# Optimization experiments

Measured on AMD Instinct MI355X. Metric: run time of the kernel, lower is better.

The kernel has to match this reference:

```python
import jax, jax.numpy as jnp
import numpy as np

LUT_DIM = 33  # standard 33^3 color LUT


def setup_inputs() -> dict:
    key = jax.random.key(0)
    k1, k2 = jax.random.split(key)
    # learned 3D LUT: [out_channels=3, D_b, D_g, D_r]
    lut = jax.random.normal(k1, (3, LUT_DIM, LUT_DIM, LUT_DIM), dtype=jnp.float32) * 0.1
    # input image batch in [0, 1): [B, 3, H, W]
    x = jax.random.uniform(k2, (4, 3, 1024, 1024), dtype=jnp.float32)
    return {"lut": lut, "x": x}


def reference(lut, x):
    """Trilinear interpolation of a 3D color LUT (image-adaptive-3DLUT forward).

    lut: [3, D, D, D] laid out as lut[c, ib, ig, ir] (flat index ir + ig*D + ib*D*D)
    x:   [B, 3, H, W] with channels (r, g, b) in [0, 1]
    returns: [B, 3, H, W]
    """
    dim = lut.shape[-1]
    scale = dim - 1  # 1 / binsize

    r, g, b = x[:, 0], x[:, 1], x[:, 2]  # each [B, H, W]

    def cell(c):
        s = c * scale
        idx = jnp.clip(jnp.floor(s), 0, scale - 1).astype(jnp.int32)
        return idx, s - idx.astype(s.dtype)  # integer cell, fractional offset

    ir, dr = cell(r)
    ig, dg = cell(g)
    ib, db = cell(b)

    lut_flat = lut.reshape(3, -1)  # [3, D^3], tiny and cache-resident

    out = jnp.zeros((3,) + r.shape, dtype=x.dtype)  # [3, B, H, W]
    # 8 corners of the enclosing LUT cell, trilinear weights
    for or_ in (0, 1):
        wr = dr if or_ else (1.0 - dr)
        for og in (0, 1):
            wg = dg if og else (1.0 - dg)
            for ob in (0, 1):
                wb = db if ob else (1.0 - db)
                flat = ((ib + ob) * dim + (ig + og)) * dim + (ir + or_)  # [B, H, W]
                corner = lut_flat[:, flat]  # gather -> [3, B, H, W]
                out = out + (wr * wg * wb)[None] * corner

    return jnp.transpose(out, (1, 0, 2, 3))  # [B, 3, H, W]
```

## Files before the change

kernel.cpp:

```cpp
#include <hip/hip_runtime.h>


#define LUT_D      33
#define LUT_DD     (LUT_D * LUT_D)
#define LUT_N      (LUT_D * LUT_D * LUT_D)
#define HW4        (1024 * 1024 / 4)
#define NGROUPS    (4 * HW4)
#define NCHUNKS    256
#define THREADS    1024
#define ITERS      (NGROUPS / NCHUNKS / THREADS)
#define STAGE_FULL 8984
#define LDS_FLOATS 35940

typedef float vfloat4 __attribute__((ext_vector_type(4)));

__global__ __launch_bounds__(THREADS)
void lut3d_trilerp_kernel(const float* __restrict__ lut,
                          const float* __restrict__ x,
                          float* __restrict__ out) {
    extern __shared__ __align__(16) float P[];

    const int bx   = blockIdx.x;
    const int xcd   = bx & 7;
    const int c     = (bx >> 3) % 3;
    const int chunk = (bx / 24) * 8 + xcd;

    const int f0  = c * LUT_N;
    const int off = f0 & 3;
    const float* ga = lut + (f0 - off);

    for (int s = 0; s < 9; ++s) {
        const int gid = s * THREADS + (int)threadIdx.x;
        if (gid < STAGE_FULL) {
            __builtin_amdgcn_global_load_lds(
                (const __attribute__((address_space(1))) void*)(ga + gid * 4),
                (__attribute__((address_space(3))) void*)(P + gid * 4),
                16, 0, 0);
        }
    }
    if (threadIdx.x < 3) {
        P[STAGE_FULL * 4 + threadIdx.x] = ga[STAGE_FULL * 4 + threadIdx.x];
    }
    __syncthreads();

    const float* L = P + off;

    const float4* x4 = (const float4*)x;
    float4*       o4 = (float4*)out;

    const int g0 = chunk * (NGROUPS / NCHUNKS) + (int)threadIdx.x;

    float4 R[ITERS], G[ITERS], B[ITERS];
    int obase[ITERS];
#pragma unroll
    for (int it = 0; it < ITERS; ++it) {
        const int g     = g0 + it * THREADS;
        const int b_img = g >> 18;
        const int hw4   = g & (HW4 - 1);
        const int ibase = b_img * 3 * HW4 + hw4;
        R[it] = x4[ibase];
        G[it] = x4[ibase + HW4];
        B[it] = x4[ibase + 2 * HW4];
        obase[it] = ibase + c * HW4;
    }

#pragma unroll
    for (int it = 0; it < ITERS; ++it) {
        const float rr[4] = {R[it].x, R[it].y, R[it].z, R[it].w};
        const float gg[4] = {G[it].x, G[it].y, G[it].z, G[it].w};
        const float bb[4] = {B[it].x, B[it].y, B[it].z, B[it].w};

        int   idx[4];
        float dr[4], dg[4], db[4];
#pragma unroll
        for (int k = 0; k < 4; ++k) {
            const float sr = rr[k] * 32.0f;
            const float sg = gg[k] * 32.0f;
            const float sb = bb[k] * 32.0f;
            const float fr = fminf(fmaxf(floorf(sr), 0.0f), 31.0f);
            const float fg = fminf(fmaxf(floorf(sg), 0.0f), 31.0f);
            const float fb = fminf(fmaxf(floorf(sb), 0.0f), 31.0f);
            dr[k] = sr - fr;
            dg[k] = sg - fg;
            db[k] = sb - fb;
            idx[k] = ((int)fb * LUT_D + (int)fg) * LUT_D + (int)fr;
        }

        float c000[4], c001[4], c010[4], c011[4];
        float c100[4], c101[4], c110[4], c111[4];
#pragma unroll
        for (int k = 0; k < 4; ++k) {
            const float* p = L + idx[k];
            c000[k] = p[0];
            c001[k] = p[1];
            c010[k] = p[LUT_D];
            c011[k] = p[LUT_D + 1];
            c100[k] = p[LUT_DD];
            c101[k] = p[LUT_DD + 1];
            c110[k] = p[LUT_DD + LUT_D];
            c111[k] = p[LUT_DD + LUT_D + 1];
        }

        float oo[4];
#pragma unroll
        for (int k = 0; k < 4; ++k) {
            const float l00 = c000[k] + dr[k] * (c001[k] - c000[k]);
            const float l01 = c010[k] + dr[k] * (c011[k] - c010[k]);
            const float l10 = c100[k] + dr[k] * (c101[k] - c100[k]);
            const float l11 = c110[k] + dr[k] * (c111[k] - c110[k]);
            const float l0  = l00 + dg[k] * (l01 - l00);
            const float l1  = l10 + dg[k] * (l11 - l10);
            oo[k] = l0 + db[k] * (l1 - l0);
        }

        vfloat4 v = {oo[0], oo[1], oo[2], oo[3]};
        __builtin_nontemporal_store(v, (vfloat4*)&o4[obase[it]]);
    }
}

extern "C" void kernel_launch(void* const* d_in, const int* in_sizes, int n_in,
                              void* d_out, int out_size, void* d_ws, size_t ws_size,
                              hipStream_t stream) {
    const float* lut = (const float*)d_in[0];
    const float* x   = (const float*)d_in[1];
    float*       out = (float*)d_out;
    (void)d_ws; (void)ws_size;

    const int grid = 3 * NCHUNKS;
    const size_t lds_bytes = LDS_FLOATS * sizeof(float);
    lut3d_trilerp_kernel<<<grid, THREADS, lds_bytes, stream>>>(lut, x, out);
}
```

Before: 117.1 us.

## Loop over output channels per block with fp16-pair packed LUT in LDS

Each block now reads its pixels once and loops over all three output channels instead of launching one block per channel. This cuts the input reads to a third. For each channel the LUT is repacked into LDS as half2 pairs (entry i, i+1), so each corner pair needs one 32-bit LDS read, four reads per pixel instead of eight. The cost is fp16 rounding of the LUT values, which changes numerics slightly. It also adds three serial LUT staging phases with barriers per block and keeps per-pixel indices and weights live in registers across channels.

```diff
diff --git a/kernel.cpp b/kernel.cpp
--- a/kernel.cpp
+++ b/kernel.cpp
@@ -1,4 +1,5 @@
 #include <hip/hip_runtime.h>
+#include <hip/hip_fp16.h>
 
 
 #define LUT_D      33
@@ -9,69 +10,49 @@
 #define NCHUNKS    256
 #define THREADS    1024
 #define ITERS      (NGROUPS / NCHUNKS / THREADS)
-#define STAGE_FULL 8984
-#define LDS_FLOATS 35940
+#define PACK_ROUNDS ((LUT_N + THREADS - 1) / THREADS)
 
 typedef float vfloat4 __attribute__((ext_vector_type(4)));
+
+__device__ __forceinline__ unsigned int pack2(float a, float b) {
+    union { __half2 h; unsigned int u; } cv;
+    cv.h = __floats2half2_rn(a, b);
+    return cv.u;
+}
+__device__ __forceinline__ float2 unpack2(unsigned int p) {
+    union { unsigned int u; __half2 h; } cv;
+    cv.u = p;
+    return __half22float2(cv.h);
+}
 
 __global__ __launch_bounds__(THREADS)
 void lut3d_trilerp_kernel(const float* __restrict__ lut,
                           const float* __restrict__ x,
                           float* __restrict__ out) {
-    extern __shared__ __align__(16) float P[];
+    extern __shared__ __align__(16) unsigned int W[];
 
-    const int bx   = blockIdx.x;
-    const int xcd   = bx & 7;
-    const int c     = (bx >> 3) % 3;
-    const int chunk = (bx / 24) * 8 + xcd;
-
-    const int f0  = c * LUT_N;
-    const int off = f0 & 3;
-    const float* ga = lut + (f0 - off);
-
-    for (int s = 0; s < 9; ++s) {
-        const int gid = s * THREADS + (int)threadIdx.x;
-        if (gid < STAGE_FULL) {
-            __builtin_amdgcn_global_load_lds(
-                (const __attribute__((address_space(1))) void*)(ga + gid * 4),
-                (__attribute__((address_space(3))) void*)(P + gid * 4),
-                16, 0, 0);
-        }
-    }
-    if (threadIdx.x < 3) {
-        P[STAGE_FULL * 4 + threadIdx.x] = ga[STAGE_FULL * 4 + threadIdx.x];
-    }
-    __syncthreads();
-
-    const float* L = P + off;
+    const int t     = (int)threadIdx.x;
+    const int chunk = blockIdx.x;
 
     const float4* x4 = (const float4*)x;
     float4*       o4 = (float4*)out;
+    const int g0 = chunk * (NGROUPS / NCHUNKS) + t;
 
-    const int g0 = chunk * (NGROUPS / NCHUNKS) + (int)threadIdx.x;
-
-    float4 R[ITERS], G[ITERS], B[ITERS];
-    int obase[ITERS];
+    int   ibase[ITERS];
+    int   idx[ITERS][4];
+    float dr[ITERS][4], dg[ITERS][4], db[ITERS][4];
 #pragma unroll
     for (int it = 0; it < ITERS; ++it) {
         const int g     = g0 + it * THREADS;
         const int b_img = g >> 18;
         const int hw4   = g & (HW4 - 1);
-        const int ibase = b_img * 3 * HW4 + hw4;
-        R[it] = x4[ibase];
-        G[it] = x4[ibase + HW4];
-        B[it] = x4[ibase + 2 * HW4];
-        obase[it] = ibase + c * HW4;
-    }
-
-#pragma unroll
-    for (int it = 0; it < ITERS; ++it) {
-        const float rr[4] = {R[it].x, R[it].y, R[it].z, R[it].w};
-        const float gg[4] = {G[it].x, G[it].y, G[it].z, G[it].w};
-        const float bb[4] = {B[it].x, B[it].y, B[it].z, B[it].w};
-
-        int   idx[4];
-        float dr[4], dg[4], db[4];
+        ibase[it] = b_img * 3 * HW4 + hw4;
+        const float4 R = x4[ibase[it]];
+        const float4 G = x4[ibase[it] + HW4];
+        const float4 B = x4[ibase[it] + 2 * HW4];
+        const float rr[4] = {R.x, R.y, R.z, R.w};
+        const float gg[4] = {G.x, G.y, G.z, G.w};
+        const float bb[4] = {B.x, B.y, B.z, B.w};
 #pragma unroll
         for (int k = 0; k < 4; ++k) {
             const float sr = rr[k] * 32.0f;
@@ -80,41 +61,57 @@
             const float fr = fminf(fmaxf(floorf(sr), 0.0f), 31.0f);
             const float fg = fminf(fmaxf(floorf(sg), 0.0f), 31.0f);
             const float fb = fminf(fmaxf(floorf(sb), 0.0f), 31.0f);
-            dr[k] = sr - fr;
-            dg[k] = sg - fg;
-            db[k] = sb - fb;
-            idx[k] = ((int)fb * LUT_D + (int)fg) * LUT_D + (int)fr;
+            dr[it][k] = sr - fr;
+            dg[it][k] = sg - fg;
+            db[it][k] = sb - fb;
+            idx[it][k] = ((int)fb * LUT_D + (int)fg) * LUT_D + (int)fr;
         }
+    }
 
-        float c000[4], c001[4], c010[4], c011[4];
-        float c100[4], c101[4], c110[4], c111[4];
+    for (int c = 0; c < 3; ++c) {
+        if (c) __syncthreads();
+
+        const float* Lc = lut + c * LUT_N;
+#pragma unroll 4
+        for (int r = 0; r < PACK_ROUNDS; ++r) {
+            const int i = r * THREADS + t;
+            if (i < LUT_N) {
+                const float a = Lc[i];
+                const float b = (i + 1 < LUT_N) ? Lc[i + 1] : 0.0f;
+                W[i] = pack2(a, b);
+            }
+        }
+        __syncthreads();
+
 #pragma unroll
-        for (int k = 0; k < 4; ++k) {
-            const float* p = L + idx[k];
-            c000[k] = p[0];
-            c001[k] = p[1];
-            c010[k] = p[LUT_D];
-            c011[k] = p[LUT_D + 1];
-            c100[k] = p[LUT_DD];
-            c101[k] = p[LUT_DD + 1];
-            c110[k] = p[LUT_DD + LUT_D];
-            c111[k] = p[LUT_DD + LUT_D + 1];
+        for (int it = 0; it < ITERS; ++it) {
+            unsigned int qA[4], qB[4], qC[4], qD[4];
+#pragma unroll
+            for (int k = 0; k < 4; ++k) {
+                const int i0 = idx[it][k];
+                qA[k] = W[i0];
+                qB[k] = W[i0 + LUT_D];
+                qC[k] = W[i0 + LUT_DD];
+                qD[k] = W[i0 + LUT_DD + LUT_D];
+            }
+            float oo[4];
+#pragma unroll
+            for (int k = 0; k < 4; ++k) {
+                const float2 a00 = unpack2(qA[k]);
+                const float2 a01 = unpack2(qB[k]);
+                const float2 a10 = unpack2(qC[k]);
+                const float2 a11 = unpack2(qD[k]);
+                const float l00 = a00.x + dr[it][k] * (a00.y - a00.x);
+                const float l01 = a01.x + dr[it][k] * (a01.y - a01.x);
+                const float l10 = a10.x + dr[it][k] * (a10.y - a10.x);
+                const float l11 = a11.x + dr[it][k] * (a11.y - a11.x);
+                const float l0  = l00 + dg[it][k] * (l01 - l00);
+                const float l1  = l10 + dg[it][k] * (l11 - l10);
+                oo[k] = l0 + db[it][k] * (l1 - l0);
+            }
+            vfloat4 v = {oo[0], oo[1], oo[2], oo[3]};
+            __builtin_nontemporal_store(v, (vfloat4*)&o4[ibase[it] + c * HW4]);
         }
-
-        float oo[4];
-#pragma unroll
-        for (int k = 0; k < 4; ++k) {
-            const float l00 = c000[k] + dr[k] * (c001[k] - c000[k]);
-            const float l01 = c010[k] + dr[k] * (c011[k] - c010[k]);
-            const float l10 = c100[k] + dr[k] * (c101[k] - c100[k]);
-            const float l11 = c110[k] + dr[k] * (c111[k] - c110[k]);
-            const float l0  = l00 + dg[k] * (l01 - l00);
-            const float l1  = l10 + dg[k] * (l11 - l10);
-            oo[k] = l0 + db[k] * (l1 - l0);
-        }
-
-        vfloat4 v = {oo[0], oo[1], oo[2], oo[3]};
-        __builtin_nontemporal_store(v, (vfloat4*)&o4[obase[it]]);
     }
 }
 
@@ -126,7 +123,6 @@
     float*       out = (float*)d_out;
     (void)d_ws; (void)ws_size;
 
-    const int grid = 3 * NCHUNKS;
-    const size_t lds_bytes = LDS_FLOATS * sizeof(float);
-    lut3d_trilerp_kernel<<<grid, THREADS, lds_bytes, stream>>>(lut, x, out);
+    const size_t lds_bytes = (size_t)LUT_N * 4;
+    lut3d_trilerp_kernel<<<NCHUNKS, THREADS, lds_bytes, stream>>>(lut, x, out);
 }
```

Measured after the change: 128.1 us. 9.4% more time.
